# Optimization experiments

Hardware: AMD Instinct MI355X
Metric: run time of the kernel (lower is better)

The kernel has to match this reference:

```python
import jax, jax.numpy as jnp
import numpy as np

THRESHOLD = 1.0
DECAY = 0.9
REFRACTORY = 2.0

B, I, H, P, T, O = 4096, 512, 1024, 4, 32, 3


def setup_inputs() -> dict:
    key = jax.random.key(0)
    ks = jax.random.split(key, 14)
    s_enc = 1.0 / np.sqrt(I)
    s_lif = 1.0 / np.sqrt(I)
    s_sel = 1.0 / np.sqrt(I)
    s_o1 = 1.0 / np.sqrt(H)
    s_o2 = 1.0 / np.sqrt(H // 2)
    return {
        "x": jax.random.normal(ks[0], (B, I), jnp.float32),
        "noise": jax.random.uniform(ks[1], (B, T, I), jnp.float32),
        "num_steps": T,
        "enc_W": jax.random.uniform(ks[2], (I, I), jnp.float32, -s_enc, s_enc),
        "enc_b": jax.random.uniform(ks[3], (I,), jnp.float32, -s_enc, s_enc),
        "sel_W": jax.random.uniform(ks[4], (I, P), jnp.float32, -s_sel, s_sel),
        "sel_b": jax.random.uniform(ks[5], (P,), jnp.float32, -s_sel, s_sel),
        "lif_W": jax.random.uniform(ks[6], (P, I, H), jnp.float32, -s_lif, s_lif),
        "lif_b": jax.random.uniform(ks[7], (P, H), jnp.float32, -s_lif, s_lif),
        "out_W1": jax.random.uniform(ks[8], (H, H // 2), jnp.float32, -s_o1, s_o1),
        "out_b1": jax.random.uniform(ks[9], (H // 2,), jnp.float32, -s_o1, s_o1),
        "out_W2": jax.random.uniform(ks[10], (H // 2, O), jnp.float32, -s_o2, s_o2),
        "out_b2": jax.random.uniform(ks[11], (O,), jnp.float32, -s_o2, s_o2),
    }


def reference(x, noise, num_steps, enc_W, enc_b, sel_W, sel_b,
              lif_W, lif_b, out_W1, out_b1, out_W2, out_b2):
    dt = x.dtype
    # spike-rate encoding: Bernoulli(sigmoid(Wx+b)) sampled with external uniform noise
    encoded = jax.nn.sigmoid(x @ enc_W + enc_b)                 # [B, I]
    spike_train = (noise < encoded[:, None, :]).astype(dt)      # [B, T, I]
    spike_train = jnp.swapaxes(spike_train, 0, 1)               # [T, B, I]

    pathway_weights = jax.nn.softmax(x @ sel_W + sel_b, axis=-1)  # [B, P]

    b = x.shape[0]
    p, h = lif_b.shape
    mem0 = jnp.zeros((p, b, h), dt)
    ref0 = jnp.zeros((p, b, h), dt)
    acc0 = jnp.zeros((b, h), dt)

    def step(carry, sp):
        mem, ref, acc = carry
        current = jnp.einsum('bi,pih->pbh', sp, lif_W) + lif_b[:, None, :]
        mem = DECAY * mem + current
        not_ref = (ref == 0).astype(dt)
        spikes = (mem >= THRESHOLD).astype(dt) * not_ref        # [P, B, H]
        mem = mem * (1.0 - spikes)
        ref = jnp.maximum(ref - 1.0 + spikes * REFRACTORY, 0.0)
        acc = acc + jnp.einsum('pbh,bp->bh', spikes, pathway_weights)
        return (mem, ref, acc), None

    (_, _, acc), _ = jax.lax.scan(step, (mem0, ref0, acc0), spike_train)
    mean_spike_rate = acc / jnp.asarray(num_steps, dt)          # [B, H]

    hid = jax.nn.relu(mean_spike_rate @ out_W1 + out_b1)
    output = hid @ out_W2 + out_b2                              # [B, O]
    return output, pathway_weights, mean_spike_rate
```

## Files before the change

kernel.cpp:

```cpp
#include <hip/hip_runtime.h>
#include <hip/hip_bf16.h>
#include <stdint.h>
#include <cstdio>
#include <math.h>


typedef unsigned int u32;
typedef unsigned long long u64;

#define ENCT_OFF 0u
#define BITS_OFF (8u << 20)
#define CB_OFF   (16u << 20)
#define HID_OFF  (80u << 20)
#define WS_NEED  ((size_t)HID_OFF + (8u << 20))

#define OUT1_F 12288
#define OUT2_F 28672

__global__ __launch_bounds__(64) void k_genc(const float* __restrict__ x,
                                             const float* __restrict__ W,
                                             const float* __restrict__ bias,
                                             float* __restrict__ encT) {
  const int lane = threadIdx.x;
  const int bg = blockIdx.x & 63;
  const int jg = blockIdx.x >> 6;
  const int b = bg * 64 + lane;
  const int j0 = jg * 8;
  const float* xr = x + (size_t)b * 512;
  float accA[8], accB[8];
#pragma unroll
  for (int u = 0; u < 8; ++u) { accA[u] = 0.0f; accB[u] = 0.0f; }
  for (int k = 0; k < 384; ++k) {
    float xv = xr[k];
#pragma unroll
    for (int u = 0; u < 8; ++u) accA[u] = fmaf(xv, W[k * 512 + j0 + u], accA[u]);
  }
  for (int k = 384; k < 512; ++k) {
    float xv = xr[k];
#pragma unroll
    for (int u = 0; u < 8; ++u) accB[u] = fmaf(xv, W[k * 512 + j0 + u], accB[u]);
  }
#pragma unroll
  for (int u = 0; u < 8; ++u) {
    float z = __fadd_rn(__fadd_rn(accA[u], accB[u]), bias[j0 + u]);
    float ef = (float)exp(-(double)z);
    float enc = 1.0f / (1.0f + ef);
    encT[(size_t)(j0 + u) * 4096 + b] = enc;
  }
}

__global__ __launch_bounds__(64) void k_spike(const float* __restrict__ noise,
                                              const float* __restrict__ encT,
                                              u64* __restrict__ bitsT) {
  const int lane = threadIdx.x;
  const int t = blockIdx.x & 31;
  const int bw = blockIdx.x >> 5;
  const int b = bw * 64 + lane;
  const float* nr = noise + ((size_t)b * 32 + t) * 512;
  u64* dst = bitsT + ((size_t)t * 64 + bw) * 512;
  for (int i0 = 0; i0 < 512; i0 += 4) {
    float4 nv = *(const float4*)(nr + i0);
    float e0 = encT[(size_t)(i0 + 0) * 4096 + b];
    float e1 = encT[(size_t)(i0 + 1) * 4096 + b];
    float e2 = encT[(size_t)(i0 + 2) * 4096 + b];
    float e3 = encT[(size_t)(i0 + 3) * 4096 + b];
    u64 m0 = __ballot(nv.x < e0);
    u64 m1 = __ballot(nv.y < e1);
    u64 m2 = __ballot(nv.z < e2);
    u64 m3 = __ballot(nv.w < e3);
    if (lane == 0) {
      dst[i0 + 0] = m0; dst[i0 + 1] = m1; dst[i0 + 2] = m2; dst[i0 + 3] = m3;
    }
  }
}

__global__ __launch_bounds__(256) void k_sel(const float* __restrict__ x,
                                             const float* __restrict__ selW,
                                             const float* __restrict__ selB,
                                             float* __restrict__ out1) {
  int b = blockIdx.x * 256 + threadIdx.x;
  const float* xr = x + (size_t)b * 512;
  double a0 = 0, a1 = 0, a2 = 0, a3 = 0;
  for (int k = 0; k < 512; ++k) {
    double xv = (double)xr[k];
    float4 w = *(const float4*)(selW + k * 4);
    a0 = fma(xv, (double)w.x, a0);
    a1 = fma(xv, (double)w.y, a1);
    a2 = fma(xv, (double)w.z, a2);
    a3 = fma(xv, (double)w.w, a3);
  }
  a0 += (double)selB[0]; a1 += (double)selB[1];
  a2 += (double)selB[2]; a3 += (double)selB[3];
  double m = fmax(fmax(a0, a1), fmax(a2, a3));
  double e0 = exp(a0 - m), e1 = exp(a1 - m), e2 = exp(a2 - m), e3 = exp(a3 - m);
  double inv = 1.0 / (e0 + e1 + e2 + e3);
  float4 wf = {(float)(e0 * inv), (float)(e1 * inv), (float)(e2 * inv), (float)(e3 * inv)};
  *(float4*)(out1 + (size_t)b * 4) = wf;
}

__global__ __launch_bounds__(64) void k_lif(const float* __restrict__ W,
                                            const float* __restrict__ lifB,
                                            const u64* __restrict__ bitsT,
                                            u32* __restrict__ cb) {
  const int lane = threadIdx.x;
  const int bid = blockIdx.x;
  const int slab = (bid & 7) * 32 + ((bid >> 3) & 31);
  const int bw = bid >> 8;
  const int p = slab >> 6;
  const int h0 = (slab & 63) * 16;
  const int b0 = bw * 64;
  const float* Wp = W + (size_t)p * 512 * 1024 + h0;
  const float* biasp = lifB + p * 1024 + h0;

  float mem[16], acc[16];
  u32 cbits[16];
  float bias_r[16];
#pragma unroll
  for (int h = 0; h < 16; ++h) {
    mem[h] = 0.0f; acc[h] = 0.0f; cbits[h] = 0u;
    bias_r[h] = biasp[h];
  }

#pragma unroll 1
  for (int t = 0; t < 32; ++t) {
    const u64* bt = bitsT + ((size_t)t * 64 + bw) * 512;
#pragma unroll 4
    for (int i = 0; i < 512; ++i) {
      u64 m = bt[i];
      float spf;
      asm("v_cndmask_b32 %0, 0, 1.0, %1" : "=v"(spf) : "s"(m));
      const float* wrow = Wp + (size_t)i * 1024;
#pragma unroll
      for (int h = 0; h < 16; ++h) acc[h] = fmaf(wrow[h], spf, acc[h]);
    }
#pragma unroll
    for (int h = 0; h < 16; ++h) {
      float c = __fadd_rn(acc[h], bias_r[h]);
      float mo = mem[h];
      bool blocked = (__float_as_uint(mo) == 0x80000000u);
      float mn = __fadd_rn(__fmul_rn(mo, 0.9f), c);
      bool sp = (mn >= 1.0f) && (!blocked);
      mem[h] = sp ? -0.0f : mn;
      cbits[h] |= (sp ? 1u : 0u) << t;
      acc[h] = 0.0f;
    }
  }
  u32* dst = cb + ((size_t)p * 4096 + b0 + lane) * 1024 + h0;
#pragma unroll
  for (int q = 0; q < 4; ++q) {
    uint4 v = {cbits[q * 4 + 0], cbits[q * 4 + 1], cbits[q * 4 + 2], cbits[q * 4 + 3]};
    *(uint4*)(dst + q * 4) = v;
  }
}

__global__ __launch_bounds__(256) void k_reduce(const u32* __restrict__ cb,
                                                const float* __restrict__ w,
                                                float* __restrict__ msr) {
  int idx = blockIdx.x * 256 + threadIdx.x;
  int h = idx & 1023;
  int b = idx >> 10;
  float4 wv = *(const float4*)(w + (size_t)b * 4);
  u32 c0 = cb[((size_t)0 * 4096 + b) * 1024 + h];
  u32 c1 = cb[((size_t)1 * 4096 + b) * 1024 + h];
  u32 c2 = cb[((size_t)2 * 4096 + b) * 1024 + h];
  u32 c3 = cb[((size_t)3 * 4096 + b) * 1024 + h];
  float acc = 0.0f;
#pragma unroll
  for (int t = 0; t < 32; ++t) {
    float s = ((c0 >> t) & 1u) ? wv.x : 0.0f;
    s = __fadd_rn(s, ((c1 >> t) & 1u) ? wv.y : 0.0f);
    s = __fadd_rn(s, ((c2 >> t) & 1u) ? wv.z : 0.0f);
    s = __fadd_rn(s, ((c3 >> t) & 1u) ? wv.w : 0.0f);
    acc = __fadd_rn(acc, s);
  }
  msr[(size_t)b * 1024 + h] = acc * 0.03125f;
}

__global__ __launch_bounds__(256) void k_gemm_relu(const float* __restrict__ A, int lda,
                                                   const float* __restrict__ W, int ldw,
                                                   const float* __restrict__ bias,
                                                   float* __restrict__ out, int ldo, int K) {
  __shared__ float As[16][65];
  __shared__ float Bs[16][64];
  const int tid = threadIdx.x;
  const int tx = tid & 15, ty = tid >> 4;
  const int n0 = blockIdx.x * 64, m0 = blockIdx.y * 64;
  const int sm = tid >> 2, skq = tid & 3;
  float acc[4][4] = {};
  for (int k0 = 0; k0 < K; k0 += 16) {
    float4 av = *(const float4*)(A + (size_t)(m0 + sm) * lda + k0 + skq * 4);
    As[skq * 4 + 0][sm] = av.x;
    As[skq * 4 + 1][sm] = av.y;
    As[skq * 4 + 2][sm] = av.z;
    As[skq * 4 + 3][sm] = av.w;
#pragma unroll
    for (int j = 0; j < 4; ++j) {
      int k = j * 4 + (tid >> 6);
      int n = tid & 63;
      Bs[k][n] = W[(size_t)(k0 + k) * ldw + n0 + n];
    }
    __syncthreads();
#pragma unroll
    for (int k = 0; k < 16; ++k) {
      float a[4], bb[4];
#pragma unroll
      for (int i = 0; i < 4; ++i) a[i] = As[k][ty * 4 + i];
#pragma unroll
      for (int i = 0; i < 4; ++i) bb[i] = Bs[k][tx * 4 + i];
#pragma unroll
      for (int i = 0; i < 4; ++i)
#pragma unroll
        for (int ii = 0; ii < 4; ++ii) acc[i][ii] = fmaf(a[i], bb[ii], acc[i][ii]);
    }
    __syncthreads();
  }
#pragma unroll
  for (int i = 0; i < 4; ++i)
#pragma unroll
    for (int ii = 0; ii < 4; ++ii) {
      float v = fmaxf(acc[i][ii] + bias[n0 + tx * 4 + ii], 0.0f);
      out[(size_t)(m0 + ty * 4 + i) * ldo + n0 + tx * 4 + ii] = v;
    }
}

__global__ __launch_bounds__(256) void k_head2(const float* __restrict__ hid,
                                               const float* __restrict__ W2,
                                               const float* __restrict__ b2,
                                               float* __restrict__ out0) {
  __shared__ float w2s[512][3];
  int tid = threadIdx.x;
  for (int i = tid; i < 1536; i += 256) ((float*)w2s)[i] = W2[i];
  __syncthreads();
  int b = blockIdx.x * 256 + tid;
  const float* hr = hid + (size_t)b * 512;
  float a0 = 0, a1 = 0, a2 = 0;
  for (int j = 0; j < 512; ++j) {
    float h = hr[j];
    a0 = fmaf(h, w2s[j][0], a0);
    a1 = fmaf(h, w2s[j][1], a1);
    a2 = fmaf(h, w2s[j][2], a2);
  }
  out0[b * 3 + 0] = a0 + b2[0];
  out0[b * 3 + 1] = a1 + b2[1];
  out0[b * 3 + 2] = a2 + b2[2];
}

extern "C" void kernel_launch(void* const* d_in, const int* in_sizes, int n_in,
                              void* d_out, int out_size, void* d_ws, size_t ws_size,
                              hipStream_t stream) {
  const float* x = (const float*)d_in[0];
  const float* noise = (const float*)d_in[1];
  const float* encW = (const float*)d_in[3];
  const float* encB = (const float*)d_in[4];
  const float* selW = (const float*)d_in[5];
  const float* selB = (const float*)d_in[6];
  const float* lifW = (const float*)d_in[7];
  const float* lifB = (const float*)d_in[8];
  const float* W1 = (const float*)d_in[9];
  const float* b1 = (const float*)d_in[10];
  const float* W2 = (const float*)d_in[11];
  const float* b2 = (const float*)d_in[12];
  float* out = (float*)d_out;
  unsigned char* ws = (unsigned char*)d_ws;

  if (ws_size < WS_NEED) {
    fprintf(stderr, "kernel_launch: ws too small (%zu < %zu)\n", ws_size, (size_t)WS_NEED);
    return;
  }

  float* encT = (float*)(ws + ENCT_OFF);
  u64* bitsT = (u64*)(ws + BITS_OFF);
  u32* cb = (u32*)(ws + CB_OFF);
  float* hid = (float*)(ws + HID_OFF);

  k_genc<<<dim3(4096), 64, 0, stream>>>(x, encW, encB, encT);
  k_sel<<<dim3(16), 256, 0, stream>>>(x, selW, selB, out + OUT1_F);
  k_spike<<<dim3(2048), 64, 0, stream>>>(noise, encT, bitsT);
  k_lif<<<dim3(16384), 64, 0, stream>>>(lifW, lifB, bitsT, cb);
  k_reduce<<<dim3(16384), 256, 0, stream>>>(cb, out + OUT1_F, out + OUT2_F);
  k_gemm_relu<<<dim3(8, 64), 256, 0, stream>>>(out + OUT2_F, 1024, W1, 512, b1, hid, 512, 1024);
  k_head2<<<dim3(16), 256, 0, stream>>>(hid, W2, b2, out);
}
```

Measured before the change: 6.822 ms.

## Register-block LIF over 8 timesteps with repacked weights and spike masks

```diff
diff --git a/kernel.cpp b/kernel.cpp
--- a/kernel.cpp
+++ b/kernel.cpp
@@ -10,8 +10,9 @@
 
 #define ENCT_OFF 0u
 #define BITS_OFF (8u << 20)
-#define CB_OFF   (16u << 20)
-#define HID_OFF  (80u << 20)
+#define WT_OFF   (16u << 20)
+#define CB_OFF   (24u << 20)
+#define HID_OFF  (88u << 20)
 #define WS_NEED  ((size_t)HID_OFF + (8u << 20))
 
 #define OUT1_F 12288
@@ -51,13 +52,13 @@
 
 __global__ __launch_bounds__(64) void k_spike(const float* __restrict__ noise,
                                               const float* __restrict__ encT,
-                                              u64* __restrict__ bitsT) {
+                                              u64* __restrict__ bitsP) {
   const int lane = threadIdx.x;
   const int t = blockIdx.x & 31;
   const int bw = blockIdx.x >> 5;
   const int b = bw * 64 + lane;
   const float* nr = noise + ((size_t)b * 32 + t) * 512;
-  u64* dst = bitsT + ((size_t)t * 64 + bw) * 512;
+  u64* dst = bitsP + (((size_t)bw * 4 + (t >> 3)) * 512) * 8 + (t & 7);
   for (int i0 = 0; i0 < 512; i0 += 4) {
     float4 nv = *(const float4*)(nr + i0);
     float e0 = encT[(size_t)(i0 + 0) * 4096 + b];
@@ -69,9 +70,24 @@
     u64 m2 = __ballot(nv.z < e2);
     u64 m3 = __ballot(nv.w < e3);
     if (lane == 0) {
-      dst[i0 + 0] = m0; dst[i0 + 1] = m1; dst[i0 + 2] = m2; dst[i0 + 3] = m3;
-    }
-  }
+      dst[(i0 + 0) * 8] = m0; dst[(i0 + 1) * 8] = m1;
+      dst[(i0 + 2) * 8] = m2; dst[(i0 + 3) * 8] = m3;
+    }
+  }
+}
+
+__global__ __launch_bounds__(256) void k_wrep(const float* __restrict__ lifW,
+                                              float* __restrict__ Wt) {
+  int idx = blockIdx.x * 256 + threadIdx.x;
+  int i = idx & 511;
+  int hs = (idx >> 9) & 127;
+  int p = idx >> 16;
+  const float* src = lifW + ((size_t)(p * 512 + i)) * 1024 + hs * 8;
+  float4 a = *(const float4*)src;
+  float4 c = *(const float4*)(src + 4);
+  float* dst = Wt + (((size_t)(p * 128 + hs)) * 512 + (size_t)i) * 8;
+  *(float4*)dst = a;
+  *(float4*)(dst + 4) = c;
 }
 
 __global__ __launch_bounds__(256) void k_sel(const float* __restrict__ x,
@@ -98,59 +114,74 @@
   *(float4*)(out1 + (size_t)b * 4) = wf;
 }
 
-__global__ __launch_bounds__(64) void k_lif(const float* __restrict__ W,
-                                            const float* __restrict__ lifB,
-                                            const u64* __restrict__ bitsT,
-                                            u32* __restrict__ cb) {
+__global__ __launch_bounds__(64, 4) void k_lif(const float* __restrict__ Wt,
+                                               const float* __restrict__ lifB,
+                                               const u64* __restrict__ bitsP,
+                                               u32* __restrict__ cb) {
   const int lane = threadIdx.x;
   const int bid = blockIdx.x;
-  const int slab = (bid & 7) * 32 + ((bid >> 3) & 31);
-  const int bw = bid >> 8;
-  const int p = slab >> 6;
-  const int h0 = (slab & 63) * 16;
+  const int xcd = bid & 7;
+  const int idx = bid >> 3;
+  const int slab = xcd * 64 + (idx & 63);
+  const int bw = idx >> 6;
+  const int p = slab >> 7;
+  const int h0 = (slab & 127) * 8;
   const int b0 = bw * 64;
-  const float* Wp = W + (size_t)p * 512 * 1024 + h0;
+  const float* wbase = Wt + (size_t)slab * 512 * 8;
+  const u64* mbase = bitsP + ((size_t)bw * 4) * 512 * 8;
   const float* biasp = lifB + p * 1024 + h0;
 
-  float mem[16], acc[16];
-  u32 cbits[16];
-  float bias_r[16];
-#pragma unroll
-  for (int h = 0; h < 16; ++h) {
-    mem[h] = 0.0f; acc[h] = 0.0f; cbits[h] = 0u;
+  float mem[8], bias_r[8];
+  u32 cbits[8];
+#pragma unroll
+  for (int h = 0; h < 8; ++h) {
+    mem[h] = 0.0f; cbits[h] = 0u;
     bias_r[h] = biasp[h];
   }
 
 #pragma unroll 1
-  for (int t = 0; t < 32; ++t) {
-    const u64* bt = bitsT + ((size_t)t * 64 + bw) * 512;
-#pragma unroll 4
+  for (int tg = 0; tg < 4; ++tg) {
+    float acc[8][8];
+#pragma unroll
+    for (int tt = 0; tt < 8; ++tt)
+#pragma unroll
+      for (int h = 0; h < 8; ++h) acc[tt][h] = 0.0f;
+
+    const u64* mrow = mbase + (size_t)tg * 512 * 8;
+#pragma unroll 2
     for (int i = 0; i < 512; ++i) {
-      u64 m = bt[i];
-      float spf;
-      asm("v_cndmask_b32 %0, 0, 1.0, %1" : "=v"(spf) : "s"(m));
-      const float* wrow = Wp + (size_t)i * 1024;
-#pragma unroll
-      for (int h = 0; h < 16; ++h) acc[h] = fmaf(wrow[h], spf, acc[h]);
-    }
-#pragma unroll
-    for (int h = 0; h < 16; ++h) {
-      float c = __fadd_rn(acc[h], bias_r[h]);
-      float mo = mem[h];
-      bool blocked = (__float_as_uint(mo) == 0x80000000u);
-      float mn = __fadd_rn(__fmul_rn(mo, 0.9f), c);
-      bool sp = (mn >= 1.0f) && (!blocked);
-      mem[h] = sp ? -0.0f : mn;
-      cbits[h] |= (sp ? 1u : 0u) << t;
-      acc[h] = 0.0f;
+      const float* wr = wbase + (size_t)i * 8;
+      const u64* mr = mrow + (size_t)i * 8;
+      float spf[8];
+#pragma unroll
+      for (int tt = 0; tt < 8; ++tt)
+        asm("v_cndmask_b32 %0, 0, 1.0, %1" : "=v"(spf[tt]) : "s"(mr[tt]));
+#pragma unroll
+      for (int tt = 0; tt < 8; ++tt)
+#pragma unroll
+        for (int h = 0; h < 8; ++h)
+          acc[tt][h] = fmaf(wr[h], spf[tt], acc[tt][h]);
+    }
+#pragma unroll
+    for (int tt = 0; tt < 8; ++tt) {
+      const int t = tg * 8 + tt;
+#pragma unroll
+      for (int h = 0; h < 8; ++h) {
+        float c = __fadd_rn(acc[tt][h], bias_r[h]);
+        float mo = mem[h];
+        bool blocked = (__float_as_uint(mo) == 0x80000000u);
+        float mn = __fadd_rn(__fmul_rn(mo, 0.9f), c);
+        bool sp = (mn >= 1.0f) && (!blocked);
+        mem[h] = sp ? -0.0f : mn;
+        cbits[h] |= (sp ? 1u : 0u) << t;
+      }
     }
   }
   u32* dst = cb + ((size_t)p * 4096 + b0 + lane) * 1024 + h0;
-#pragma unroll
-  for (int q = 0; q < 4; ++q) {
-    uint4 v = {cbits[q * 4 + 0], cbits[q * 4 + 1], cbits[q * 4 + 2], cbits[q * 4 + 3]};
-    *(uint4*)(dst + q * 4) = v;
-  }
+  uint4 v0 = {cbits[0], cbits[1], cbits[2], cbits[3]};
+  uint4 v1 = {cbits[4], cbits[5], cbits[6], cbits[7]};
+  *(uint4*)dst = v0;
+  *(uint4*)(dst + 4) = v1;
 }
 
 __global__ __launch_bounds__(256) void k_reduce(const u32* __restrict__ cb,
@@ -269,14 +300,16 @@
   }
 
   float* encT = (float*)(ws + ENCT_OFF);
-  u64* bitsT = (u64*)(ws + BITS_OFF);
+  u64* bitsP = (u64*)(ws + BITS_OFF);
+  float* Wt = (float*)(ws + WT_OFF);
   u32* cb = (u32*)(ws + CB_OFF);
   float* hid = (float*)(ws + HID_OFF);
 
   k_genc<<<dim3(4096), 64, 0, stream>>>(x, encW, encB, encT);
   k_sel<<<dim3(16), 256, 0, stream>>>(x, selW, selB, out + OUT1_F);
-  k_spike<<<dim3(2048), 64, 0, stream>>>(noise, encT, bitsT);
-  k_lif<<<dim3(16384), 64, 0, stream>>>(lifW, lifB, bitsT, cb);
+  k_wrep<<<dim3(1024), 256, 0, stream>>>(lifW, Wt);
+  k_spike<<<dim3(2048), 64, 0, stream>>>(noise, encT, bitsP);
+  k_lif<<<dim3(32768), 64, 0, stream>>>(Wt, lifB, bitsP, cb);
   k_reduce<<<dim3(16384), 256, 0, stream>>>(cb, out + OUT1_F, out + OUT2_F);
   k_gemm_relu<<<dim3(8, 64), 256, 0, stream>>>(out + OUT2_F, 1024, W1, 512, b1, hid, 512, 1024);
   k_head2<<<dim3(16), 256, 0, stream>>>(hid, W2, b2, out);
```

Result: slower. 7.937 ms (+16.3%).
